# Performance work log

Hardware: AMD Instinct MI355X
Metric: run time of the kernel (lower is better)

Reference implementation:

```python
import jax, jax.numpy as jnp
import numpy as np


def setup_inputs() -> dict:
    key = jax.random.key(0)
    k1, k2, k3, k4 = jax.random.split(key, 4)
    B, H, W, C = 4, 64, 64, 512
    x = jax.random.normal(k1, (B, H, W, C), dtype=jnp.float32)
    Wb = jax.random.normal(k2, (C, C // 8), dtype=jnp.float32) * 0.05
    Wc = jax.random.normal(k3, (C, C // 8), dtype=jnp.float32) * 0.05
    Wd = jax.random.normal(k4, (C, C), dtype=jnp.float32) * 0.05
    gamma = jnp.ones((1,), dtype=jnp.float32)
    return {"x": x, "Wb": Wb, "Wc": Wc, "Wd": Wd, "gamma": gamma}


def reference(x, Wb, Wc, Wd, gamma):
    B, H, W, C = x.shape
    hw = H * W
    xf = x.reshape(B, hw, C)                      # [B, hw, C]
    b = jnp.einsum('bnc,ck->bnk', xf, Wb)         # key   [B, hw, C/8]
    c = jnp.einsum('bnc,ck->bnk', xf, Wc)         # query [B, hw, C/8]
    d = jnp.einsum('bnc,cf->bnf', xf, Wd)         # value [B, hw, C]
    # attention energy: c @ b^T, softmax over last axis (keras default)
    energy = jnp.einsum('bqk,bnk->bqn', c, b)     # [B, hw, hw]
    attn = jax.nn.softmax(energy, axis=-1)
    out = jnp.einsum('bqn,bnf->bqf', attn, d)     # [B, hw, C]
    out = out.reshape(B, H, W, C)
    return gamma * out + x
```

## Files before the change

kernel.cpp:

```cpp
#include <hip/hip_runtime.h>
#include <hip/hip_bf16.h>
#include <stdint.h>

typedef __attribute__((ext_vector_type(8))) short short8;
typedef __attribute__((ext_vector_type(4))) float f32x4;
typedef _Float16 half8 __attribute__((ext_vector_type(8)));

#define LOG2E 1.4426950408889634f
#define SHIFT2 100.98865286222744f

__device__ __forceinline__ unsigned short f2bf(float f) {
  union { float f; unsigned u; } v; v.f = f;
  unsigned u = v.u;
  unsigned r = u + 0x7FFF + ((u >> 16) & 1);
  return (unsigned short)(r >> 16);
}
__device__ __forceinline__ float bf2f(unsigned short h) {
  union { unsigned u; float f; } v; v.u = ((unsigned)h) << 16; return v.f;
}

__global__ void convert_x_kernel(const float* __restrict__ x,
                                 unsigned short* __restrict__ xh,
                                 _Float16* __restrict__ xf, int n4) {
  int i = blockIdx.x * blockDim.x + threadIdx.x;
  if (i >= n4) return;
  float4 v = ((const float4*)x)[i];
  ushort4 h;
  h.x = f2bf(v.x); h.y = f2bf(v.y); h.z = f2bf(v.z); h.w = f2bf(v.w);
  union { _Float16 f[4]; ushort4 u; } p;
  p.f[0] = (_Float16)v.x; p.f[1] = (_Float16)v.y;
  p.f[2] = (_Float16)v.z; p.f[3] = (_Float16)v.w;
  ((ushort4*)xh)[i] = h;
  ((ushort4*)xf)[i] = p.u;
}

__global__ void prep_w_kernel(const float* __restrict__ Wb,
                              const float* __restrict__ Wc,
                              const float* __restrict__ Wd,
                              _Float16* __restrict__ wf,
                              unsigned short* __restrict__ whd) {
  int gid = blockIdx.x * 256 + threadIdx.x;
  int n = gid >> 9, k = gid & 511;
  if (n < 128) {
    float v = (n < 64) ? Wb[k * 64 + n] : Wc[k * 64 + (n - 64)];
    wf[n * 512 + k] = (_Float16)v;
  } else {
    whd[(size_t)(n - 128) * 512 + k] = f2bf(Wd[k * 512 + (n - 128)]);
  }
}

__launch_bounds__(256)
__global__ void proj_gemm_kernel(const unsigned short* __restrict__ xh,
                                 const _Float16* __restrict__ xf,
                                 const unsigned short* __restrict__ whd,
                                 const _Float16* __restrict__ wf,
                                 _Float16* __restrict__ bq,
                                 _Float16* __restrict__ cq,
                                 unsigned short* __restrict__ dT) {
  __shared__ unsigned short As[128 * 32];
  __shared__ unsigned short Bs[128 * 32];
  const int row0 = blockIdx.x * 128;
  const int col0 = blockIdx.y * 128;
  const bool bc = (blockIdx.y == 0);
  const int w = threadIdx.x >> 6;
  const int lane = threadIdx.x & 63;
  const int wm = (w >> 1) * 64, wn = (w & 1) * 64;
  const int quad = lane >> 4, m16 = lane & 15;
  const int lrow = lane >> 2, lseg = lane & 3;

  const unsigned short* asrc = bc ? (const unsigned short*)xf : xh;
  const unsigned short* bsrc = bc ? (const unsigned short*)wf : whd;
  const int bcol0 = bc ? 0 : (col0 - 128);

  const f32x4 fzero = {0.f, 0.f, 0.f, 0.f};
  f32x4 acc[4][4];
  for (int i = 0; i < 4; i++)
    for (int j = 0; j < 4; j++) acc[i][j] = fzero;

  for (int k0 = 0; k0 < 512; k0 += 32) {
    for (int i = 0; i < 2; i++) {
      int r = (w * 2 + i) * 16 + lrow;
      size_t aoff = (size_t)(row0 + r) * 512 + k0 + lseg * 8;
      size_t boff = (size_t)(bcol0 + r) * 512 + k0 + lseg * 8;
      int loff = r * 32 + lseg * 8;
      __builtin_amdgcn_global_load_lds(
          (const __attribute__((address_space(1))) unsigned int*)(asrc + aoff),
          (__attribute__((address_space(3))) unsigned int*)(As + loff), 16, 0, 0);
      __builtin_amdgcn_global_load_lds(
          (const __attribute__((address_space(1))) unsigned int*)(bsrc + boff),
          (__attribute__((address_space(3))) unsigned int*)(Bs + loff), 16, 0, 0);
    }
    __syncthreads();
    if (bc) {
      half8 ah[4], bh[4];
      for (int mt = 0; mt < 4; mt++)
        ah[mt] = *(const half8*)(As + (wm + mt * 16 + m16) * 32 + quad * 8);
      for (int nt = 0; nt < 4; nt++)
        bh[nt] = *(const half8*)(Bs + (wn + nt * 16 + m16) * 32 + quad * 8);
      for (int mt = 0; mt < 4; mt++)
        for (int nt = 0; nt < 4; nt++)
          acc[mt][nt] = __builtin_amdgcn_mfma_f32_16x16x32_f16(ah[mt], bh[nt],
                                                               acc[mt][nt], 0, 0, 0);
    } else {
      short8 ah[4], bh[4];
      for (int mt = 0; mt < 4; mt++)
        ah[mt] = *(const short8*)(As + (wm + mt * 16 + m16) * 32 + quad * 8);
      for (int nt = 0; nt < 4; nt++)
        bh[nt] = *(const short8*)(Bs + (wn + nt * 16 + m16) * 32 + quad * 8);
      for (int mt = 0; mt < 4; mt++)
        for (int nt = 0; nt < 4; nt++)
          acc[mt][nt] = __builtin_amdgcn_mfma_f32_16x16x32_bf16(ah[mt], bh[nt],
                                                                acc[mt][nt], 0, 0, 0);
    }
    __syncthreads();
  }

  for (int mt = 0; mt < 4; mt++) {
    int rowb = row0 + wm + mt * 16 + quad * 4;
    for (int nt = 0; nt < 4; nt++) {
      int n = wn + nt * 16 + m16;
      f32x4 v = acc[mt][nt];
      if (bc) {
        _Float16* dst = (n < 64) ? bq : cq;
        int nn = n & 63;
        for (int r = 0; r < 4; r++)
          dst[(size_t)(rowb + r) * 64 + nn] = (_Float16)v[r];
      } else {
        int f = col0 - 128 + n;
        int batch = rowb >> 12, tok = rowb & 4095;
        ushort4 o;
        o.x = f2bf(v[0]); o.y = f2bf(v[1]); o.z = f2bf(v[2]); o.w = f2bf(v[3]);
        *(ushort4*)(dT + ((size_t)batch * 512 + f) * 4096 + tok) = o;
      }
    }
  }
}

#define PSTR 72

__launch_bounds__(256, 3)
__global__ void attn_kernel(const _Float16* __restrict__ bq,
                            const _Float16* __restrict__ cq,
                            const unsigned short* __restrict__ dT,
                            float* __restrict__ O0,
                            float* __restrict__ O1,
                            float* __restrict__ lbuf) {
  __shared__ unsigned short p_lds[2][64 * PSTR];

  const int batch = blockIdx.y;
  const int split = blockIdx.z;
  const int fhalf = blockIdx.x >> 6;
  const int q0 = (blockIdx.x & 63) * 64;
  const int tid = threadIdx.x;
  const int w = tid >> 6, lane = tid & 63;
  const int quad = lane >> 4, m16 = lane & 15;
  const int colc = w * 16 + m16;
  const int f0 = fhalf * 256 + w * 64;

  const _Float16* cb = cq + ((size_t)batch * 4096 + q0) * 64;
  const _Float16* kb = bq + (size_t)batch * 4096 * 64;
  const unsigned short* vb = dT + (size_t)batch * 512 * 4096;
  float* Op = split ? O1 : O0;

  half8 qf[4][2];
  for (int mt = 0; mt < 4; mt++)
    for (int ks = 0; ks < 2; ks++)
      qf[mt][ks] = *(const half8*)(cb + (size_t)(mt * 16 + m16) * 64 +
                                   ks * 32 + quad * 8);

  const f32x4 fzero = {0.f, 0.f, 0.f, 0.f};
  f32x4 acc[4][4];
  for (int i = 0; i < 4; i++)
    for (int j = 0; j < 4; j++) acc[i][j] = fzero;

  const int sq = tid >> 2, sseg = tid & 3;
  float psum = 0.0f;

  const int kt0 = split * 32, kt1 = kt0 + 32;

  auto qk_step = [&](int kti, int nbuf) {
    const _Float16* kp = kb + ((size_t)kti * 64 + colc) * 64 + quad * 8;
    half8 K0 = *(const half8*)(kp);
    half8 K1 = *(const half8*)(kp + 32);
    for (int mt = 0; mt < 4; mt++) {
      f32x4 s = __builtin_amdgcn_mfma_f32_16x16x32_f16(qf[mt][0], K0, fzero, 0, 0, 0);
      s = __builtin_amdgcn_mfma_f32_16x16x32_f16(qf[mt][1], K1, s, 0, 0, 0);
      int rbase = mt * 16 + quad * 4;
#pragma unroll
      for (int r = 0; r < 4; r++) {
        float p = __builtin_amdgcn_exp2f(fmaf(s[r], LOG2E, -SHIFT2));
        p_lds[nbuf][(rbase + r) * PSTR + colc] = f2bf(p);
      }
    }
  };

  qk_step(kt0, 0);
  __syncthreads();

  for (int kt = kt0; kt < kt1; kt++) {
    const int buf = kt & 1;

    short8 vf0[4];
#pragma unroll
    for (int ft = 0; ft < 4; ft++)
      vf0[ft] = *(const short8*)(vb + (size_t)(f0 + ft * 16 + m16) * 4096 +
                                 kt * 64 + quad * 8);

    if (kt + 1 < kt1) qk_step(kt + 1, buf ^ 1);

    short8 vf1[4];
#pragma unroll
    for (int ft = 0; ft < 4; ft++)
      vf1[ft] = *(const short8*)(vb + (size_t)(f0 + ft * 16 + m16) * 4096 +
                                 kt * 64 + 32 + quad * 8);

    if (fhalf == 0) {
      const unsigned short* pr = p_lds[buf] + sq * PSTR + sseg * 16;
      short8 a = *(const short8*)(pr);
      short8 b = *(const short8*)(pr + 8);
      float ps = 0.f;
#pragma unroll
      for (int i = 0; i < 8; i++)
        ps += bf2f((unsigned short)a[i]) + bf2f((unsigned short)b[i]);
      psum += ps;
    }

    for (int ks = 0; ks < 2; ks++) {
      short8 pf[4];
      for (int mt = 0; mt < 4; mt++)
        pf[mt] = *(const short8*)(p_lds[buf] + (mt * 16 + m16) * PSTR +
                                  ks * 32 + quad * 8);
      const short8* vv = ks ? vf1 : vf0;
      for (int ft = 0; ft < 4; ft++)
        for (int mt = 0; mt < 4; mt++)
          acc[mt][ft] = __builtin_amdgcn_mfma_f32_16x16x32_bf16(pf[mt], vv[ft],
                                                                acc[mt][ft], 0, 0, 0);
    }
    __syncthreads();
  }

  if (fhalf == 0) {
    psum += __shfl_xor(psum, 1);
    psum += __shfl_xor(psum, 2);
    if (sseg == 0)
      lbuf[(size_t)split * 16384 + batch * 4096 + (q0 + sq)] = psum;
  }
  for (int mt = 0; mt < 4; mt++) {
    for (int ft = 0; ft < 4; ft++) {
      int f = f0 + ft * 16 + m16;
      for (int r = 0; r < 4; r++) {
        int row = q0 + mt * 16 + quad * 4 + r;
        Op[((size_t)batch * 4096 + row) * 512 + f] = acc[mt][ft][r];
      }
    }
  }
}

__global__ void combine_kernel(const float* __restrict__ O0,
                               const float* __restrict__ O1,
                               const float* __restrict__ lbuf,
                               const float* __restrict__ x,
                               const float* __restrict__ gamma,
                               float* __restrict__ out) {
  int gid = blockIdx.x * 256 + threadIdx.x;
  int row = gid >> 7;
  float rl = 1.0f / (lbuf[row] + lbuf[16384 + row]);
  float g = gamma[0];
  float4 o0 = ((const float4*)O0)[gid];
  float4 o1 = ((const float4*)O1)[gid];
  float4 xv = ((const float4*)x)[gid];
  float4 r;
  r.x = g * ((o0.x + o1.x) * rl) + xv.x;
  r.y = g * ((o0.y + o1.y) * rl) + xv.y;
  r.z = g * ((o0.z + o1.z) * rl) + xv.z;
  r.w = g * ((o0.w + o1.w) * rl) + xv.w;
  ((float4*)out)[gid] = r;
}

extern "C" void kernel_launch(void* const* d_in, const int* in_sizes, int n_in,
                              void* d_out, int out_size, void* d_ws, size_t ws_size,
                              hipStream_t stream) {
  (void)in_sizes; (void)n_in; (void)out_size; (void)ws_size;
  const float* x = (const float*)d_in[0];
  const float* Wb = (const float*)d_in[1];
  const float* Wc = (const float*)d_in[2];
  const float* Wd = (const float*)d_in[3];
  const float* gamma = (const float*)d_in[4];
  float* out = (float*)d_out;

  unsigned short* ws = (unsigned short*)d_ws;
  unsigned short* xh  = ws;
  _Float16* xf  = (_Float16*)(ws + 8388608);
  unsigned short* whd = ws + 16777216;
  _Float16* wf  = (_Float16*)(ws + 17039360);
  _Float16* bqp = (_Float16*)(ws + 17104896);
  _Float16* cqp = (_Float16*)(ws + 18153472);
  unsigned short* dT  = ws + 19202048;
  float* lb = (float*)(ws + 27590656);
  float* Opart0 = out;
  float* Opart1 = (float*)ws;

  convert_x_kernel<<<8192, 256, 0, stream>>>(x, xh, xf, 2097152);
  prep_w_kernel<<<1280, 256, 0, stream>>>(Wb, Wc, Wd, wf, whd);
  proj_gemm_kernel<<<dim3(128, 5), 256, 0, stream>>>(xh, xf, whd, wf,
                                                     bqp, cqp, dT);
  attn_kernel<<<dim3(128, 4, 2), 256, 0, stream>>>(bqp, cqp, dT,
                                                   Opart0, Opart1, lb);
  combine_kernel<<<8192, 256, 0, stream>>>(Opart0, Opart1, lb, x, gamma, out);
}
```

Before: 307.2 us.

## Drop split-K in attention and fuse normalization and residual epilogue

Removes the two-way split over key tiles so each block runs all 64 key tiles. Row sums are reduced in shared memory and the 1/l scaling, gamma and residual add happen in the attention epilogue, so the combine kernel and the two partial-output buffers go away. The cost is half as many blocks (512 instead of 1024), each with twice the serial work, and launch bounds are relaxed to two blocks per SM. Every block now also computes the row sums, not just the fhalf==0 blocks.

```diff
diff --git a/kernel.cpp b/kernel.cpp
--- a/kernel.cpp
+++ b/kernel.cpp
@@ -138,17 +138,17 @@
 
 #define PSTR 72
 
-__launch_bounds__(256, 3)
+__launch_bounds__(256, 2)
 __global__ void attn_kernel(const _Float16* __restrict__ bq,
                             const _Float16* __restrict__ cq,
                             const unsigned short* __restrict__ dT,
-                            float* __restrict__ O0,
-                            float* __restrict__ O1,
-                            float* __restrict__ lbuf) {
+                            const float* __restrict__ x,
+                            const float* __restrict__ gamma,
+                            float* __restrict__ out) {
   __shared__ unsigned short p_lds[2][64 * PSTR];
+  __shared__ float lsum[64];
 
   const int batch = blockIdx.y;
-  const int split = blockIdx.z;
   const int fhalf = blockIdx.x >> 6;
   const int q0 = (blockIdx.x & 63) * 64;
   const int tid = threadIdx.x;
@@ -160,7 +160,7 @@
   const _Float16* cb = cq + ((size_t)batch * 4096 + q0) * 64;
   const _Float16* kb = bq + (size_t)batch * 4096 * 64;
   const unsigned short* vb = dT + (size_t)batch * 512 * 4096;
-  float* Op = split ? O1 : O0;
+  const float g0 = gamma[0];
 
   half8 qf[4][2];
   for (int mt = 0; mt < 4; mt++)
@@ -175,8 +175,6 @@
 
   const int sq = tid >> 2, sseg = tid & 3;
   float psum = 0.0f;
-
-  const int kt0 = split * 32, kt1 = kt0 + 32;
 
   auto qk_step = [&](int kti, int nbuf) {
     const _Float16* kp = kb + ((size_t)kti * 64 + colc) * 64 + quad * 8;
@@ -194,10 +192,10 @@
     }
   };
 
-  qk_step(kt0, 0);
+  qk_step(0, 0);
   __syncthreads();
 
-  for (int kt = kt0; kt < kt1; kt++) {
+  for (int kt = 0; kt < 64; kt++) {
     const int buf = kt & 1;
 
     short8 vf0[4];
@@ -206,7 +204,7 @@
       vf0[ft] = *(const short8*)(vb + (size_t)(f0 + ft * 16 + m16) * 4096 +
                                  kt * 64 + quad * 8);
 
-    if (kt + 1 < kt1) qk_step(kt + 1, buf ^ 1);
+    if (kt + 1 < 64) qk_step(kt + 1, buf ^ 1);
 
     short8 vf1[4];
 #pragma unroll
@@ -214,7 +212,7 @@
       vf1[ft] = *(const short8*)(vb + (size_t)(f0 + ft * 16 + m16) * 4096 +
                                  kt * 64 + 32 + quad * 8);
 
-    if (fhalf == 0) {
+    {
       const unsigned short* pr = p_lds[buf] + sq * PSTR + sseg * 16;
       short8 a = *(const short8*)(pr);
       short8 b = *(const short8*)(pr + 8);
@@ -239,42 +237,27 @@
     __syncthreads();
   }
 
-  if (fhalf == 0) {
-    psum += __shfl_xor(psum, 1);
-    psum += __shfl_xor(psum, 2);
-    if (sseg == 0)
-      lbuf[(size_t)split * 16384 + batch * 4096 + (q0 + sq)] = psum;
-  }
+  psum += __shfl_xor(psum, 1);
+  psum += __shfl_xor(psum, 2);
+  if (sseg == 0) lsum[sq] = psum;
+  __syncthreads();
+
+  const float* xp = x + ((size_t)batch * 4096 + q0) * 512;
+  float* op = out + ((size_t)batch * 4096 + q0) * 512;
   for (int mt = 0; mt < 4; mt++) {
+    float rlv[4];
+#pragma unroll
+    for (int r = 0; r < 4; r++)
+      rlv[r] = 1.0f / lsum[mt * 16 + quad * 4 + r];
     for (int ft = 0; ft < 4; ft++) {
       int f = f0 + ft * 16 + m16;
+#pragma unroll
       for (int r = 0; r < 4; r++) {
-        int row = q0 + mt * 16 + quad * 4 + r;
-        Op[((size_t)batch * 4096 + row) * 512 + f] = acc[mt][ft][r];
+        size_t o = (size_t)(mt * 16 + quad * 4 + r) * 512 + f;
+        op[o] = g0 * (acc[mt][ft][r] * rlv[r]) + xp[o];
       }
     }
   }
-}
-
-__global__ void combine_kernel(const float* __restrict__ O0,
-                               const float* __restrict__ O1,
-                               const float* __restrict__ lbuf,
-                               const float* __restrict__ x,
-                               const float* __restrict__ gamma,
-                               float* __restrict__ out) {
-  int gid = blockIdx.x * 256 + threadIdx.x;
-  int row = gid >> 7;
-  float rl = 1.0f / (lbuf[row] + lbuf[16384 + row]);
-  float g = gamma[0];
-  float4 o0 = ((const float4*)O0)[gid];
-  float4 o1 = ((const float4*)O1)[gid];
-  float4 xv = ((const float4*)x)[gid];
-  float4 r;
-  r.x = g * ((o0.x + o1.x) * rl) + xv.x;
-  r.y = g * ((o0.y + o1.y) * rl) + xv.y;
-  r.z = g * ((o0.z + o1.z) * rl) + xv.z;
-  r.w = g * ((o0.w + o1.w) * rl) + xv.w;
-  ((float4*)out)[gid] = r;
 }
 
 extern "C" void kernel_launch(void* const* d_in, const int* in_sizes, int n_in,
@@ -296,15 +279,10 @@
   _Float16* bqp = (_Float16*)(ws + 17104896);
   _Float16* cqp = (_Float16*)(ws + 18153472);
   unsigned short* dT  = ws + 19202048;
-  float* lb = (float*)(ws + 27590656);
-  float* Opart0 = out;
-  float* Opart1 = (float*)ws;
 
   convert_x_kernel<<<8192, 256, 0, stream>>>(x, xh, xf, 2097152);
   prep_w_kernel<<<1280, 256, 0, stream>>>(Wb, Wc, Wd, wf, whd);
   proj_gemm_kernel<<<dim3(128, 5), 256, 0, stream>>>(xh, xf, whd, wf,
                                                      bqp, cqp, dT);
-  attn_kernel<<<dim3(128, 4, 2), 256, 0, stream>>>(bqp, cqp, dT,
-                                                   Opart0, Opart1, lb);
-  combine_kernel<<<8192, 256, 0, stream>>>(Opart0, Opart1, lb, x, gamma, out);
-}
+  attn_kernel<<<dim3(128, 4), 256, 0, stream>>>(bqp, cqp, dT, x, gamma, out);
+}
```

New measurement: 282.6 us. -8.0%, faster.
